# Performance work log

Hardware: AMD Instinct MI355X
Metric: run time of the kernel (lower is better)

Reference implementation:

```python
import jax, jax.numpy as jnp
import numpy as np

NTYPES = 2
B, N, MNEI = 4, 512, 100
M = MNEI * NTYPES          # neighbor slots = maxNeighborNum * ntypes
EMB_LAST = 100             # embedding net sizes [25, 50, 100]
FIT_H = 240
M2 = 16
RMIN, RMAX = 0.5, 6.0


def setup_inputs():
    key = jax.random.key(0)
    ks = jax.random.split(key, 24)
    r = jax.random.uniform(ks[0], (B, N, M), minval=0.6, maxval=7.0)
    v = jax.random.normal(ks[1], (B, N, M, 3))
    v = v / jnp.linalg.norm(v, axis=-1, keepdims=True)
    keep = jax.random.uniform(ks[2], (B, N, M)) < 0.7
    ImageDR = jnp.concatenate([r[..., None], r[..., None] * v], axis=-1)
    ImageDR = jnp.where(keep[..., None], ImageDR, 0.0).astype(jnp.float32)
    Imagetype_map = jax.random.randint(ks[3], (N,), 0, NTYPES)
    list_neigh = jax.random.randint(ks[4], (B, N, M), 0, N + 1)
    type_map = jnp.arange(NTYPES)
    davg = (0.01 * jax.random.normal(ks[5], (NTYPES, M, 4))).astype(jnp.float32)
    dstd = (1.0 + 0.1 * jax.random.uniform(ks[6], (NTYPES, M, 4))).astype(jnp.float32)

    def w(k, shape, fan):
        return (jax.random.normal(k, shape) / np.sqrt(fan)).astype(jnp.float32)

    def b(k, shape):
        return (0.1 * jax.random.normal(k, shape)).astype(jnp.float32)

    emb_W0 = w(ks[7], (NTYPES, NTYPES, 1, 25), 1)
    emb_b0 = b(ks[8], (NTYPES, NTYPES, 25))
    emb_W1 = w(ks[9], (NTYPES, NTYPES, 25, 50), 25)
    emb_b1 = b(ks[10], (NTYPES, NTYPES, 50))
    emb_W2 = w(ks[11], (NTYPES, NTYPES, 50, 100), 50)
    emb_b2 = b(ks[12], (NTYPES, NTYPES, 100))
    fin = M2 * EMB_LAST
    fit_W0 = w(ks[13], (NTYPES, fin, FIT_H), fin)
    fit_b0 = b(ks[14], (NTYPES, FIT_H))
    fit_W1 = w(ks[15], (NTYPES, FIT_H, FIT_H), FIT_H)
    fit_b1 = b(ks[16], (NTYPES, FIT_H))
    fit_W2 = w(ks[17], (NTYPES, FIT_H, FIT_H), FIT_H)
    fit_b2 = b(ks[18], (NTYPES, FIT_H))
    fit_W3 = w(ks[19], (NTYPES, FIT_H, 1), FIT_H)
    fit_b3 = b(ks[20], (NTYPES, 1))
    energy_shift = jnp.array([-3.37, -5.21], dtype=jnp.float32)
    return dict(list_neigh=list_neigh, Imagetype_map=Imagetype_map, type_map=type_map,
                ImageDR=ImageDR, nghost=0, davg=davg, dstd=dstd,
                emb_W0=emb_W0, emb_b0=emb_b0, emb_W1=emb_W1, emb_b1=emb_b1,
                emb_W2=emb_W2, emb_b2=emb_b2,
                fit_W0=fit_W0, fit_b0=fit_b0, fit_W1=fit_W1, fit_b1=fit_b1,
                fit_W2=fit_W2, fit_b2=fit_b2, fit_W3=fit_W3, fit_b3=fit_b3,
                energy_shift=energy_shift)


def _emb(s, W0, b0, W1, b1, W2, b2):
    # DeepPot-SE embedding net with doubling resnet connections
    h = jnp.tanh(s @ W0 + b0)                                   # [..., 25]
    h = jnp.tanh(h @ W1 + b1) + jnp.concatenate([h, h], -1)     # [..., 50]
    return jnp.tanh(h @ W2 + b2) + jnp.concatenate([h, h], -1)  # [..., 100]


def _fit(d, W0, b0, W1, b1, W2, b2, W3, b3):
    h = jnp.tanh(d @ W0 + b0)
    h = h + jnp.tanh(h @ W1 + b1)
    h = h + jnp.tanh(h @ W2 + b2)
    return h @ W3 + b3


def _forward(ImageDR, davg, dstd,
             emb_W0, emb_b0, emb_W1, emb_b1, emb_W2, emb_b2,
             fit_W0, fit_b0, fit_W1, fit_b1, fit_W2, fit_b2, fit_W3, fit_b3,
             energy_shift, Imagetype_map):
    Bsz, Nat, Mtot, _ = ImageDR.shape
    m = Mtot // NTYPES
    R = ImageDR[..., 0]
    Rsafe = jnp.where(R > 1e-5, R, 1.0)
    # smooth switching function s(r): 1/r below Rmin, polynomial taper to Rmax
    u = (R - RMIN) / (RMAX - RMIN)
    mid = (u ** 3 * (-6.0 * u * u + 15.0 * u - 10.0) + 1.0) / Rsafe
    S = jnp.where((R > 0) & (R < RMIN), 1.0 / Rsafe,
                  jnp.where((R > RMIN) & (R < RMAX), mid, 0.0))
    msk = (jnp.abs(R) > 1e-5)[..., None]
    Ri = jnp.concatenate([S[..., None],
                          jnp.where(msk, (S / Rsafe)[..., None] * ImageDR[..., 1:4], 0.0)],
                         axis=-1)                                    # [B,N,M,4] = (s, s*x/r, s*y/r, s*z/r)
    # per-center-type normalization (irregular gather of stats)
    Rn = (Ri - davg[Imagetype_map][None]) / dstd[Imagetype_map][None]
    tmask = [(Imagetype_map == i).astype(Rn.dtype)[None, :, None, None] for i in range(NTYPES)]
    xyz = jnp.zeros((Bsz, Nat, 4, EMB_LAST), Rn.dtype)
    for j in range(NTYPES):                                          # neighbor-type slice
        sl = Rn[:, :, j * m:(j + 1) * m, :]                          # [B,N,m,4]
        s = sl[..., 0:1]
        G = jnp.zeros(sl.shape[:3] + (EMB_LAST,), sl.dtype)
        for i in range(NTYPES):                                      # center type -> pair net (i, j)
            G = G + tmask[i] * _emb(s, emb_W0[i, j], emb_b0[i, j],
                                    emb_W1[i, j], emb_b1[i, j], emb_W2[i, j], emb_b2[i, j])
        xyz = xyz + jnp.einsum('bnmk,bnmc->bnkc', sl, G)
    xyz = xyz / (m * NTYPES)
    # descriptor D = (Ri^T G)^T (Ri^T G)[:, :M2], flattened -> [B,N,EMB_LAST*M2]
    D = jnp.einsum('bnkc,bnkd->bncd', xyz, xyz[..., :M2]).reshape(Bsz, Nat, -1)
    Ei = jnp.zeros((Bsz, Nat), D.dtype)
    for i in range(NTYPES):
        e = _fit(D, fit_W0[i], fit_b0[i], fit_W1[i], fit_b1[i],
                 fit_W2[i], fit_b2[i], fit_W3[i], fit_b3[i])[..., 0] + energy_shift[i]
        Ei = Ei + tmask[i][:, :, 0, 0] * e
    Etot = jnp.sum(Ei, axis=1)
    return Etot, Ei


def reference(list_neigh, Imagetype_map, type_map, ImageDR, nghost, davg, dstd,
              emb_W0, emb_b0, emb_W1, emb_b1, emb_W2, emb_b2,
              fit_W0, fit_b0, fit_W1, fit_b1, fit_W2, fit_b2, fit_W3, fit_b3,
              energy_shift):
    return _forward(ImageDR, davg, dstd,
                    emb_W0, emb_b0, emb_W1, emb_b1, emb_W2, emb_b2,
                    fit_W0, fit_b0, fit_W1, fit_b1, fit_W2, fit_b2, fit_W3, fit_b3,
                    energy_shift, Imagetype_map)
```

## Files before the change

### kernel.cpp

```cpp
#include <hip/hip_runtime.h>
#include <math.h>

#define NT 2
#define BSZ 4
#define NAT 512
#define NATOMS 2048
#define NNEI 200
#define EMB 100
#define FITH 240
#define DDIM 1600
#define TBK 1024

#define BIAS_F  16
#define W3C_F   (BIAS_F + 3 * 512)
#define PERM_I  2064
#define CNT_I   (PERM_I + 2064)
#define IPERM_I (CNT_I + 4)
#define DONE_I  (IPERM_I + 2048)
#define USH_BYTE 24832
#define TBL_U   0
#define W0T_U   409600
#define W1T_U   (W0T_U + 819200)
#define W2T_U   (W1T_U + 262144)
#define D_U     (W2T_U + 262144)
#define D_SZ    (129 * 50 * 512)
#define USH_END (D_U + D_SZ)
#define WS_NEED ((size_t)USH_BYTE + (size_t)USH_END * 2)

#define N_W0 819200
#define N_W1 262144
#define N_W2 262144
#define N_B  1536
#define N_W3 512
#define N_EI 2048
#define N_WT (N_W0 + N_W1 + N_W2 + N_B + N_W3 + N_EI)
#define WT_BLK ((N_WT + 255) / 256)
#define TB_BLK 512

#define HPAD 264
#define FIT_NBLK 256

typedef short s8v __attribute__((ext_vector_type(8)));
typedef float f4v __attribute__((ext_vector_type(4)));

__device__ __forceinline__ float ftanh(float x) {
    float ax = fabsf(x);
    float e = __expf(2.0f * ax);
    float t = 1.0f - __fdividef(2.0f, e + 1.0f);
    return (x < 0.0f) ? -t : t;
}
__device__ __forceinline__ unsigned short f2bf(float f) {
    unsigned u = __float_as_uint(f);
    u += 0x7FFFu + ((u >> 16) & 1u);
    return (unsigned short)(u >> 16);
}
__device__ __forceinline__ float bf2f(unsigned short s) {
    return __uint_as_float(((unsigned)s) << 16);
}
__device__ __forceinline__ float calc_S(float R) {
    float Rsafe = (R > 1e-5f) ? R : 1.0f;
    float u = (R - 0.5f) * (1.0f / 5.5f);
    float uu = u * u;
    float mid = (u * uu * (-6.0f * uu + 15.0f * u - 10.0f) + 1.0f) / Rsafe;
    float S = 0.0f;
    if (R > 0.0f && R < 0.5f)      S = 1.0f / Rsafe;
    else if (R > 0.5f && R < 6.0f) S = mid;
    return S;
}

__global__ void __launch_bounds__(256) prep_kernel(
    const float* __restrict__ fW0, const float* __restrict__ fW1,
    const float* __restrict__ fW2,
    const float* __restrict__ fb0, const float* __restrict__ fb1,
    const float* __restrict__ fb2,
    const float* __restrict__ fW3, const float* __restrict__ fb3,
    const float* __restrict__ eshift,
    const float* __restrict__ davg, const float* __restrict__ dstd,
    const float* __restrict__ eW0, const float* __restrict__ eb0,
    const float* __restrict__ eW1, const float* __restrict__ eb1,
    const float* __restrict__ eW2, const float* __restrict__ eb2,
    const int* __restrict__ itype,
    float* __restrict__ ws, float* __restrict__ out)
{
    __shared__ float los[100], his[100];
    __shared__ float rng[2];
    __shared__ float h0s[8][25];
    __shared__ float h1s[8][50];
    __shared__ int pcnt, poff0, poff1;
    const int tid = threadIdx.x;
    int bxg = blockIdx.x;
    unsigned short* u0 = (unsigned short*)((char*)ws + USH_BYTE);

    if (bxg < WT_BLK) {
        int id = bxg * 256 + tid;
        if (id < N_W0) {
            int e = id & 7, lane = (id >> 3) & 63;
            int rem = id >> 9;
            int kt = rem % 50, c16 = rem / 50;
            int n = c16 * 16 + (lane & 15);
            int k = kt * 32 + (lane >> 4) * 8 + e;
            float v = 0.0f;
            if (n < 240)                  v = fW0[(size_t)k * 240 + n];
            else if (n >= 256 && n < 496) v = fW0[(size_t)(1600 + k) * 240 + (n - 256)];
            u0[W0T_U + id] = f2bf(v);
            return;
        }
        id -= N_W0;
        if (id < N_W1) {
            int e = id & 7, lane = (id >> 3) & 63;
            int rem = id >> 9;
            int kt = rem & 15, c16 = rem >> 4;
            int n = c16 * 16 + (lane & 15);
            int k = kt * 32 + (lane >> 4) * 8 + e;
            float v = 0.0f;
            if (n < 240 && k < 240)       v = fW1[(size_t)k * 240 + n];
            else if (n >= 256 && n < 496 && k >= 256 && k < 496)
                                          v = fW1[(size_t)(240 + (k - 256)) * 240 + (n - 256)];
            u0[W1T_U + id] = f2bf(v);
            return;
        }
        id -= N_W1;
        if (id < N_W2) {
            int e = id & 7, lane = (id >> 3) & 63;
            int rem = id >> 9;
            int kt = rem & 15, c16 = rem >> 4;
            int n = c16 * 16 + (lane & 15);
            int k = kt * 32 + (lane >> 4) * 8 + e;
            float v = 0.0f;
            if (n < 240 && k < 240)       v = fW2[(size_t)k * 240 + n];
            else if (n >= 256 && n < 496 && k >= 256 && k < 496)
                                          v = fW2[(size_t)(240 + (k - 256)) * 240 + (n - 256)];
            u0[W2T_U + id] = f2bf(v);
            return;
        }
        id -= N_W2;
        if (id < N_B) {
            int l = id / 512, n = id - l * 512;
            const float* fb = (l == 0) ? fb0 : (l == 1) ? fb1 : fb2;
            float v = 0.0f;
            if (n < 240)                  v = fb[n];
            else if (n >= 256 && n < 496) v = fb[240 + (n - 256)];
            ws[BIAS_F + l * 512 + n] = v;
            return;
        }
        id -= N_B;
        if (id < N_W3) {
            int n = id;
            float v = 0.0f;
            if (n < 240)                  v = fW3[n];
            else if (n >= 256 && n < 496) v = fW3[240 + (n - 256)];
            ws[W3C_F + n] = v;
            return;
        }
        id -= N_W3;
        if (id < N_EI) {
            int t = itype[id & (NAT - 1)];
            out[4 + id] = fb3[t] + eshift[t];
        }
        return;
    }
    bxg -= WT_BLK;
    if (bxg < TB_BLK) {
        const int nid = bxg >> 7;
        const int kb  = (bxg & 127) * 8;
        const int t = nid >> 1, j = nid & 1;
        if (tid < 100) {
            int m = j * 100 + tid;
            float av = davg[(t * NNEI + m) * 4];
            float sd = dstd[(t * NNEI + m) * 4];
            float inv = __fdividef(1.0f, sd);
            float a = (0.0f - av) * inv;
            float b = (2.0f - av) * inv;
            los[tid] = fminf(a, b);
            his[tid] = fmaxf(a, b);
        }
        __syncthreads();
        if (tid == 0) {
            float lo = los[0], hi = his[0];
            for (int i = 1; i < 100; ++i) { lo = fminf(lo, los[i]); hi = fmaxf(hi, his[i]); }
            rng[0] = lo; rng[1] = hi - lo;
            if (kb == 0) {
                ws[nid * 2] = lo;
                ws[nid * 2 + 1] = (float)(TBK - 1) / (hi - lo);
            }
        }
        __syncthreads();
        const float smin = rng[0], span = rng[1];
        const float* W0 = eW0 + nid * 25;
        const float* B0 = eb0 + nid * 25;
        if (tid < 200) {
            int q = tid / 25, a = tid % 25;
            float s = smin + span * ((float)(kb + q) * (1.0f / (TBK - 1)));
            h0s[q][a] = ftanh(fmaf(s, W0[a], B0[a]));
        }
        __syncthreads();
        const float* W1 = eW1 + nid * 1250;
        const float* B1 = eb1 + nid * 50;
        for (int idx = tid; idx < 400; idx += 256) {
            int q = idx / 50, cc = idx % 50;
            float acc = B1[cc];
#pragma unroll
            for (int a = 0; a < 25; ++a) acc = fmaf(h0s[q][a], W1[a * 50 + cc], acc);
            h1s[q][cc] = ftanh(acc) + h0s[q][(cc < 25) ? cc : cc - 25];
        }
        __syncthreads();
        const float* W2 = eW2 + nid * 5000;
        const float* B2 = eb2 + nid * 100;
        unsigned short* tblu = u0 + TBL_U;
        for (int idx = tid; idx < 800; idx += 256) {
            int q = idx / 100, c = idx % 100;
            float acc = B2[c];
#pragma unroll
            for (int a = 0; a < 50; ++a) acc = fmaf(h1s[q][a], W2[a * 100 + c], acc);
            float g = ftanh(acc) + h1s[q][(c < 50) ? c : c - 50];
            tblu[(size_t)(nid * TBK + kb + q) * 100 + c] = f2bf(g);
        }
        return;
    }
    if (tid == 0) { pcnt = 0; poff0 = 0; poff1 = 0; }
    __syncthreads();
    int* wsi = (int*)ws;
    int local0 = 0;
    for (int i = tid; i < NATOMS; i += 256) local0 += (itype[i & (NAT - 1)] == 0);
    atomicAdd(&pcnt, local0);
    __syncthreads();
    const int c0 = pcnt;
    const int c0p = (c0 + 15) & ~15;
    for (int i = tid; i < NATOMS; i += 256) {
        int t = itype[i & (NAT - 1)];
        int pos = (t == 0) ? atomicAdd(&poff0, 1) : (c0p + atomicAdd(&poff1, 1));
        wsi[PERM_I + pos] = i;
        wsi[IPERM_I + i] = pos;
    }
    if (tid == 0) {
        wsi[CNT_I] = c0; wsi[CNT_I + 1] = NATOMS - c0; wsi[CNT_I + 2] = c0p;
        wsi[DONE_I] = 0;
    }
}

__global__ void __launch_bounds__(512) embed_kernel(
    const int* __restrict__ itype, const float* __restrict__ imagedr,
    const float* __restrict__ davg, const float* __restrict__ dstd,
    float* __restrict__ ws)
{
    __shared__ __align__(16) float4 srn[NNEI];
    __shared__ float sx[NNEI];
    __shared__ float part[8][400];
    const int atom = blockIdx.x;
    const int n = atom & (NAT - 1);
    const int tid = threadIdx.x;
    const int t = itype[n];
    unsigned short* u0 = (unsigned short*)((char*)ws + USH_BYTE);
    const int* wsi = (const int*)ws;

    const float sm0 = ws[(t * 2 + 0) * 2], sc0 = ws[(t * 2 + 0) * 2 + 1];
    const float sm1 = ws[(t * 2 + 1) * 2], sc1 = ws[(t * 2 + 1) * 2 + 1];

    for (int m = tid; m < NNEI; m += 512) {
        float4 dr = ((const float4*)imagedr)[(size_t)atom * NNEI + m];
        float R = dr.x;
        float S = calc_S(R);
        float Rsafe = (R > 1e-5f) ? R : 1.0f;
        float sr = (fabsf(R) > 1e-5f) ? (S / Rsafe) : 0.0f;
        float4 av = ((const float4*)davg)[t * NNEI + m];
        float4 sd = ((const float4*)dstd)[t * NNEI + m];
        float4 rv;
        rv.x = (S         - av.x) / sd.x;
        rv.y = (sr * dr.y - av.y) / sd.y;
        rv.z = (sr * dr.z - av.z) / sd.z;
        rv.w = (sr * dr.w - av.w) / sd.w;
        srn[m] = rv;
        float smin = (m >= 100) ? sm1 : sm0;
        float scal = (m >= 100) ? sc1 : sc0;
        sx[m] = fminf(fmaxf((rv.x - smin) * scal, 0.0f), (float)(TBK - 2) + 0.9999f);
    }
    __syncthreads();

    const int v = tid >> 6, lane = tid & 63;
    const int w = v >> 2;
    const int seg = v & 3;
    const unsigned short* T = u0 + TBL_U + (size_t)(t * 2 + w) * TBK * EMB;
    const bool act = (lane < 50);
    float xE0 = 0, xE1 = 0, xE2 = 0, xE3 = 0;
    float xO0 = 0, xO1 = 0, xO2 = 0, xO3 = 0;
#pragma unroll 5
    for (int mi = seg * 25; mi < seg * 25 + 25; ++mi) {
        int m = w * 100 + mi;
        float4 rv = srn[m];
        float x = sx[m];
        int i = (int)x;
        float f = x - (float)i;
        const unsigned short* Tr = T + (size_t)i * EMB;
        unsigned r0 = act ? *(const unsigned*)(Tr + 2 * lane) : 0u;
        unsigned r1 = act ? *(const unsigned*)(Tr + EMB + 2 * lane) : 0u;
        float g0e = bf2f((unsigned short)(r0 & 0xFFFFu));
        float g0o = bf2f((unsigned short)(r0 >> 16));
        float g1e = bf2f((unsigned short)(r1 & 0xFFFFu));
        float g1o = bf2f((unsigned short)(r1 >> 16));
        float ge = fmaf(f, g1e - g0e, g0e);
        float go = fmaf(f, g1o - g0o, g0o);
        xE0 = fmaf(rv.x, ge, xE0); xE1 = fmaf(rv.y, ge, xE1);
        xE2 = fmaf(rv.z, ge, xE2); xE3 = fmaf(rv.w, ge, xE3);
        xO0 = fmaf(rv.x, go, xO0); xO1 = fmaf(rv.y, go, xO1);
        xO2 = fmaf(rv.z, go, xO2); xO3 = fmaf(rv.w, go, xO3);
    }
    if (act) {
        const int c = 2 * lane;
        part[v][0 * 100 + c] = xE0; part[v][0 * 100 + c + 1] = xO0;
        part[v][1 * 100 + c] = xE1; part[v][1 * 100 + c + 1] = xO1;
        part[v][2 * 100 + c] = xE2; part[v][2 * 100 + c + 1] = xO2;
        part[v][3 * 100 + c] = xE3; part[v][3 * 100 + c + 1] = xO3;
    }
    __syncthreads();
    const float inv = 1.0f / 200.0f;
    for (int idx = tid; idx < 400; idx += 512) {
        float s = 0.0f;
#pragma unroll
        for (int pv = 0; pv < 8; ++pv) s += part[pv][idx];
        part[0][idx] = s * inv;
    }
    __syncthreads();
    const int p = wsi[IPERM_I + atom];
    const int rb = p >> 4, mrp = p & 15;
    unsigned short* Df = u0 + D_U;
    const float* xt = part[0];
    for (int k8 = tid; k8 < 200; k8 += 512) {
        int k = k8 * 8;
        int c = k >> 4, d0 = k & 15;
        int kt = k >> 5, q = (k >> 3) & 3;
        s8v pack;
#pragma unroll
        for (int e = 0; e < 8; ++e) {
            int d = d0 + e;
            float s = xt[c] * xt[d] + xt[100 + c] * xt[100 + d]
                    + xt[200 + c] * xt[200 + d] + xt[300 + c] * xt[300 + d];
            ((unsigned short*)&pack)[e] = f2bf(s);
        }
        *(s8v*)(Df + ((size_t)(rb * 50 + kt) * 64 + q * 16 + mrp) * 8) = pack;
    }
}

__global__ void __launch_bounds__(512, 2) fit_kernel(
    const unsigned short* __restrict__ Af,
    const unsigned short* __restrict__ W0F,
    const unsigned short* __restrict__ W1F,
    const unsigned short* __restrict__ W2F,
    const float* __restrict__ biases,
    const float* __restrict__ w3c,
    int* __restrict__ wsi,
    float* __restrict__ out)
{
    __shared__ float lred[4][64][17];
    __shared__ unsigned short Hs0[16 * HPAD];
    __shared__ unsigned short Hs1[16 * HPAD];
    __shared__ float red2[16][4];
    __shared__ int lastFlag;
    __shared__ float er[8];

    const int z = blockIdx.y;
    const int cnt = wsi[CNT_I + z];
    const int my = blockIdx.x;
    const int tid = threadIdx.x;
    const bool work = (my * 16 < cnt);
    if (work) {
        const int basep = z ? wsi[CNT_I + 2] : 0;
        const int w = tid >> 6, lane = tid & 63;
        const int mr = lane & 15, q = lane >> 4;
        const int wc = w & 3, h = w >> 2;
        const int n0 = z * 256 + wc * 64;
        const int m0 = my * 16;
        const int rb = (basep >> 4) + my;
        const int c16b = z * 16 + wc * 4;

        f4v a0 = {0,0,0,0}, a1 = {0,0,0,0}, a2 = {0,0,0,0}, a3 = {0,0,0,0};
        {
            const unsigned short* Ap = Af  + ((size_t)(rb * 50 + h * 25) * 64 + lane) * 8;
            const unsigned short* Bp = W0F + ((size_t)(c16b * 50 + h * 25) * 64 + lane) * 8;
#pragma unroll
            for (int kt = 0; kt < 25; ++kt) {
                s8v av = *(const s8v*)(Ap + kt * 512);
                s8v b0 = *(const s8v*)(Bp + kt * 512);
                s8v b1 = *(const s8v*)(Bp + 25600 + kt * 512);
                s8v b2 = *(const s8v*)(Bp + 51200 + kt * 512);
                s8v b3 = *(const s8v*)(Bp + 76800 + kt * 512);
                a0 = __builtin_amdgcn_mfma_f32_16x16x32_bf16(av, b0, a0, 0, 0, 0);
                a1 = __builtin_amdgcn_mfma_f32_16x16x32_bf16(av, b1, a1, 0, 0, 0);
                a2 = __builtin_amdgcn_mfma_f32_16x16x32_bf16(av, b2, a2, 0, 0, 0);
                a3 = __builtin_amdgcn_mfma_f32_16x16x32_bf16(av, b3, a3, 0, 0, 0);
            }
        }
        if (h == 1) {
#pragma unroll
            for (int r = 0; r < 4; ++r) {
                lred[wc][lane][r]      = a0[r];
                lred[wc][lane][4 + r]  = a1[r];
                lred[wc][lane][8 + r]  = a2[r];
                lred[wc][lane][12 + r] = a3[r];
            }
        }
        __syncthreads();
        if (h == 0) {
#pragma unroll
            for (int j = 0; j < 4; ++j) {
                const float bv = biases[n0 + j * 16 + mr];
                f4v* ap = (j == 0) ? &a0 : (j == 1) ? &a1 : (j == 2) ? &a2 : &a3;
                const int col = wc * 64 + j * 16 + mr;
#pragma unroll
                for (int r = 0; r < 4; ++r) {
                    float s = (*ap)[r] + lred[wc][lane][j * 4 + r] + bv;
                    int row = q * 4 + r;
                    Hs0[row * HPAD + col] = f2bf(ftanh(s));
                }
            }
        }
        __syncthreads();

        {
            const unsigned short* Bp = W1F + ((size_t)(c16b * 16 + z * 8 + h * 4) * 64 + lane) * 8;
            f4v ac[4] = {{0,0,0,0},{0,0,0,0},{0,0,0,0},{0,0,0,0}};
#pragma unroll
            for (int kt = 0; kt < 4; ++kt) {
                s8v av = *(const s8v*)((const char*)Hs0
                         + (size_t)mr * (HPAD * 2) + h * 256 + q * 16 + kt * 64);
                s8v b0 = *(const s8v*)(Bp + kt * 512);
                s8v b1 = *(const s8v*)(Bp + 8192 + kt * 512);
                s8v b2 = *(const s8v*)(Bp + 16384 + kt * 512);
                s8v b3 = *(const s8v*)(Bp + 24576 + kt * 512);
                ac[0] = __builtin_amdgcn_mfma_f32_16x16x32_bf16(av, b0, ac[0], 0, 0, 0);
                ac[1] = __builtin_amdgcn_mfma_f32_16x16x32_bf16(av, b1, ac[1], 0, 0, 0);
                ac[2] = __builtin_amdgcn_mfma_f32_16x16x32_bf16(av, b2, ac[2], 0, 0, 0);
                ac[3] = __builtin_amdgcn_mfma_f32_16x16x32_bf16(av, b3, ac[3], 0, 0, 0);
            }
            if (h == 1) {
#pragma unroll
                for (int j = 0; j < 4; ++j)
#pragma unroll
                    for (int r = 0; r < 4; ++r) lred[wc][lane][j * 4 + r] = ac[j][r];
            }
            __syncthreads();
            if (h == 0) {
#pragma unroll
                for (int j = 0; j < 4; ++j) {
                    const float bv = biases[512 + n0 + j * 16 + mr];
                    const int col = wc * 64 + j * 16 + mr;
#pragma unroll
                    for (int r = 0; r < 4; ++r) {
                        float s = ac[j][r] + lred[wc][lane][j * 4 + r] + bv;
                        int row = q * 4 + r;
                        float hv = bf2f(Hs0[row * HPAD + col]) + ftanh(s);
                        Hs1[row * HPAD + col] = f2bf(hv);
                    }
                }
            }
            __syncthreads();
        }

        {
            const unsigned short* Bp = W2F + ((size_t)(c16b * 16 + z * 8 + h * 4) * 64 + lane) * 8;
            f4v ac[4] = {{0,0,0,0},{0,0,0,0},{0,0,0,0},{0,0,0,0}};
#pragma unroll
            for (int kt = 0; kt < 4; ++kt) {
                s8v av = *(const s8v*)((const char*)Hs1
                         + (size_t)mr * (HPAD * 2) + h * 256 + q * 16 + kt * 64);
                s8v b0 = *(const s8v*)(Bp + kt * 512);
                s8v b1 = *(const s8v*)(Bp + 8192 + kt * 512);
                s8v b2 = *(const s8v*)(Bp + 16384 + kt * 512);
                s8v b3 = *(const s8v*)(Bp + 24576 + kt * 512);
                ac[0] = __builtin_amdgcn_mfma_f32_16x16x32_bf16(av, b0, ac[0], 0, 0, 0);
                ac[1] = __builtin_amdgcn_mfma_f32_16x16x32_bf16(av, b1, ac[1], 0, 0, 0);
                ac[2] = __builtin_amdgcn_mfma_f32_16x16x32_bf16(av, b2, ac[2], 0, 0, 0);
                ac[3] = __builtin_amdgcn_mfma_f32_16x16x32_bf16(av, b3, ac[3], 0, 0, 0);
            }
            if (h == 1) {
#pragma unroll
                for (int j = 0; j < 4; ++j)
#pragma unroll
                    for (int r = 0; r < 4; ++r) lred[wc][lane][j * 4 + r] = ac[j][r];
            }
            __syncthreads();
            if (h == 0) {
                float pr[4] = {0, 0, 0, 0};
#pragma unroll
                for (int j = 0; j < 4; ++j) {
                    const int col = n0 + j * 16 + mr;
                    const float bv = biases[1024 + col];
                    const float wv = w3c[col];
                    const int coll = wc * 64 + j * 16 + mr;
#pragma unroll
                    for (int r = 0; r < 4; ++r) {
                        float s = ac[j][r] + lred[wc][lane][j * 4 + r] + bv;
                        int row = q * 4 + r;
                        float hv = bf2f(Hs1[row * HPAD + coll]) + ftanh(s);
                        pr[r] = fmaf(hv, wv, pr[r]);
                    }
                }
#pragma unroll
                for (int r = 0; r < 4; ++r) {
                    float p = pr[r];
                    p += __shfl_xor(p, 1, 16);
                    p += __shfl_xor(p, 2, 16);
                    p += __shfl_xor(p, 4, 16);
                    p += __shfl_xor(p, 8, 16);
                    if (mr == 0) red2[q * 4 + r][wc] = p;
                }
            }
            __syncthreads();
            if (tid < 16 && m0 + tid < cnt) {
                const int orow = wsi[PERM_I + basep + m0 + tid];
                out[4 + orow] += red2[tid][0] + red2[tid][1] + red2[tid][2] + red2[tid][3];
            }
        }
    }

    __syncthreads();
    if (tid == 0) {
        __threadfence();
        int prev = atomicAdd(&wsi[DONE_I], 1);
        lastFlag = (prev == FIT_NBLK - 1);
    }
    __syncthreads();
    if (lastFlag) {
        __threadfence();
        const int g = tid >> 7, l = tid & 127;
        float s = 0.0f;
        for (int nn = l; nn < NAT; nn += 128) s += out[4 + g * NAT + nn];
#pragma unroll
        for (int off = 32; off > 0; off >>= 1) s += __shfl_down(s, off, 64);
        if ((l & 63) == 0) er[g * 2 + (l >> 6)] = s;
        __syncthreads();
        if (tid < 4) out[tid] = er[tid * 2] + er[tid * 2 + 1];
    }
}

__global__ void etot_kernel(float* __restrict__ out) {
    const int b = blockIdx.x;
    float s = 0.0f;
    for (int n = threadIdx.x; n < NAT; n += 256) s += out[4 + b * NAT + n];
#pragma unroll
    for (int off = 32; off > 0; off >>= 1) s += __shfl_down(s, off, 64);
    __shared__ float rr[4];
    if ((threadIdx.x & 63) == 0) rr[threadIdx.x >> 6] = s;
    __syncthreads();
    if (threadIdx.x == 0) out[b] = rr[0] + rr[1] + rr[2] + rr[3];
}

__global__ void dp_atom_kernel(
    const int* __restrict__ itype, const float* __restrict__ imagedr,
    const float* __restrict__ davg, const float* __restrict__ dstd,
    const float* __restrict__ eW0, const float* __restrict__ eb0,
    const float* __restrict__ eW1, const float* __restrict__ eb1,
    const float* __restrict__ eW2, const float* __restrict__ eb2,
    const float* __restrict__ fW0, const float* __restrict__ fb0,
    const float* __restrict__ fW1, const float* __restrict__ fb1,
    const float* __restrict__ fW2, const float* __restrict__ fb2,
    const float* __restrict__ fW3, const float* __restrict__ fb3,
    const float* __restrict__ eshift, float* __restrict__ out)
{
    __shared__ __align__(16) float4 rn4[NNEI];
    __shared__ __align__(16) float  xyz[4 * EMB];
    __shared__ __align__(16) float  h0s[100 * 25];
    __shared__ __align__(16) float  smem[100 * 52];
    const int atom = blockIdx.x;
    const int n = atom & (NAT - 1);
    const int tid = threadIdx.x;
    const int t = itype[n];
    for (int m = tid; m < NNEI; m += 256) {
        float4 dr = ((const float4*)imagedr)[(size_t)atom * NNEI + m];
        float R = dr.x;
        float S = calc_S(R);
        float Rsafe = (R > 1e-5f) ? R : 1.0f;
        float sr = (fabsf(R) > 1e-5f) ? (S / Rsafe) : 0.0f;
        float4 av = ((const float4*)davg)[t * NNEI + m];
        float4 sd = ((const float4*)dstd)[t * NNEI + m];
        float4 rv;
        rv.x = (S - av.x) / sd.x; rv.y = (sr * dr.y - av.y) / sd.y;
        rv.z = (sr * dr.z - av.z) / sd.z; rv.w = (sr * dr.w - av.w) / sd.w;
        rn4[m] = rv;
    }
    const int c = tid & 127; const int mh = tid >> 7;
    float xp0 = 0, xp1 = 0, xp2 = 0, xp3 = 0;
    for (int j = 0; j < NT; ++j) {
        const int wb = t * NT + j;
        const float* W0 = eW0 + wb * 25; const float* B0 = eb0 + wb * 25;
        const float* W1 = eW1 + wb * 1250; const float* B1 = eb1 + wb * 50;
        const float* W2 = eW2 + wb * 5000; const float* B2 = eb2 + wb * 100;
        __syncthreads();
        for (int idx = tid; idx < 2500; idx += 256) {
            int m = idx / 25, a = idx - m * 25;
            h0s[idx] = ftanh(fmaf(rn4[j * 100 + m].x, W0[a], B0[a]));
        }
        __syncthreads();
        for (int idx = tid; idx < 5000; idx += 256) {
            int m = idx / 50, cc = idx - m * 50;
            const float* h0m = h0s + m * 25;
            float acc = B1[cc];
#pragma unroll
            for (int a = 0; a < 25; ++a) acc = fmaf(h0m[a], W1[a * 50 + cc], acc);
            smem[m * 52 + cc] = ftanh(acc) + h0m[(cc < 25) ? cc : cc - 25];
        }
        for (int idx = tid; idx < 200; idx += 256)
            smem[(idx >> 1) * 52 + 50 + (idx & 1)] = 0.0f;
        __syncthreads();
        if (c < EMB) {
            float w2c[52];
#pragma unroll
            for (int a = 0; a < 50; ++a) w2c[a] = W2[a * EMB + c];
            w2c[50] = 0; w2c[51] = 0;
            const float bc = B2[c];
            const int sk = (c < 50) ? c : c - 50;
            for (int i = 0; i < 50; ++i) {
                int m = mh * 50 + i;
                const float* h1m = smem + m * 52;
                float acc = bc;
#pragma unroll
                for (int q = 0; q < 13; ++q) {
                    float4 hv = ((const float4*)h1m)[q];
                    acc = fmaf(hv.x, w2c[4 * q], acc); acc = fmaf(hv.y, w2c[4 * q + 1], acc);
                    acc = fmaf(hv.z, w2c[4 * q + 2], acc); acc = fmaf(hv.w, w2c[4 * q + 3], acc);
                }
                float g = ftanh(acc) + h1m[sk];
                float4 rm = rn4[j * 100 + m];
                xp0 = fmaf(rm.x, g, xp0); xp1 = fmaf(rm.y, g, xp1);
                xp2 = fmaf(rm.z, g, xp2); xp3 = fmaf(rm.w, g, xp3);
            }
        }
    }
    __syncthreads();
    const float inv = 1.0f / 200.0f;
    if (mh == 0 && c < EMB) {
        xyz[c] = xp0 * inv; xyz[EMB + c] = xp1 * inv;
        xyz[2 * EMB + c] = xp2 * inv; xyz[3 * EMB + c] = xp3 * inv;
    }
    __syncthreads();
    if (mh == 1 && c < EMB) {
        xyz[c] += xp0 * inv; xyz[EMB + c] += xp1 * inv;
        xyz[2 * EMB + c] += xp2 * inv; xyz[3 * EMB + c] += xp3 * inv;
    }
    __syncthreads();
    float* Dld = smem;
    for (int idx = tid; idx < DDIM; idx += 256) {
        int cc = idx >> 4, d = idx & 15;
        Dld[idx] = xyz[cc] * xyz[d] + xyz[EMB + cc] * xyz[EMB + d]
                 + xyz[2 * EMB + cc] * xyz[2 * EMB + d] + xyz[3 * EMB + cc] * xyz[3 * EMB + d];
    }
    __syncthreads();
    float* hA = smem + DDIM; float* hB = hA + FITH; float* h2 = hB + FITH; float* red = h2 + FITH;
    if (tid < FITH) {
        const float* W = fW0 + (size_t)t * DDIM * FITH;
        float acc = fb0[t * FITH + tid];
        for (int f = 0; f < DDIM; f += 4) {
            float4 dv = *(const float4*)(Dld + f);
            acc = fmaf(dv.x, W[f * FITH + tid], acc); acc = fmaf(dv.y, W[(f + 1) * FITH + tid], acc);
            acc = fmaf(dv.z, W[(f + 2) * FITH + tid], acc); acc = fmaf(dv.w, W[(f + 3) * FITH + tid], acc);
        }
        hA[tid] = ftanh(acc);
    }
    __syncthreads();
    if (tid < FITH) {
        const float* W = fW1 + t * FITH * FITH;
        float acc = fb1[t * FITH + tid];
        for (int f = 0; f < FITH; f += 4) {
            float4 hv = *(const float4*)(hA + f);
            acc = fmaf(hv.x, W[f * FITH + tid], acc); acc = fmaf(hv.y, W[(f + 1) * FITH + tid], acc);
            acc = fmaf(hv.z, W[(f + 2) * FITH + tid], acc); acc = fmaf(hv.w, W[(f + 3) * FITH + tid], acc);
        }
        hB[tid] = hA[tid] + ftanh(acc);
    }
    __syncthreads();
    if (tid < FITH) {
        const float* W = fW2 + t * FITH * FITH;
        float acc = fb2[t * FITH + tid];
        for (int f = 0; f < FITH; f += 4) {
            float4 hv = *(const float4*)(hB + f);
            acc = fmaf(hv.x, W[f * FITH + tid], acc); acc = fmaf(hv.y, W[(f + 1) * FITH + tid], acc);
            acc = fmaf(hv.z, W[(f + 2) * FITH + tid], acc); acc = fmaf(hv.w, W[(f + 3) * FITH + tid], acc);
        }
        h2[tid] = hB[tid] + ftanh(acc);
    }
    __syncthreads();
    float p = (tid < FITH) ? h2[tid] * fW3[t * FITH + tid] : 0.0f;
#pragma unroll
    for (int off = 32; off > 0; off >>= 1) p += __shfl_down(p, off, 64);
    if ((tid & 63) == 0) red[tid >> 6] = p;
    __syncthreads();
    if (tid == 0) out[4 + atom] = red[0] + red[1] + red[2] + red[3] + fb3[t] + eshift[t];
}

extern "C" void kernel_launch(void* const* d_in, const int* in_sizes, int n_in,
                              void* d_out, int out_size, void* d_ws, size_t ws_size,
                              hipStream_t stream) {
    const int*   itype   = (const int*)  d_in[1];
    const float* imagedr = (const float*)d_in[3];
    const float* davg    = (const float*)d_in[5];
    const float* dstd    = (const float*)d_in[6];
    const float* eW0     = (const float*)d_in[7];
    const float* eb0     = (const float*)d_in[8];
    const float* eW1     = (const float*)d_in[9];
    const float* eb1     = (const float*)d_in[10];
    const float* eW2     = (const float*)d_in[11];
    const float* eb2     = (const float*)d_in[12];
    const float* fW0     = (const float*)d_in[13];
    const float* fb0     = (const float*)d_in[14];
    const float* fW1     = (const float*)d_in[15];
    const float* fb1     = (const float*)d_in[16];
    const float* fW2     = (const float*)d_in[17];
    const float* fb2     = (const float*)d_in[18];
    const float* fW3     = (const float*)d_in[19];
    const float* fb3     = (const float*)d_in[20];
    const float* eshift  = (const float*)d_in[21];
    float* out = (float*)d_out;
    float* ws  = (float*)d_ws;

    if (ws_size >= WS_NEED) {
        unsigned short* u0 = (unsigned short*)((char*)ws + USH_BYTE);
        int* wsi = (int*)ws;
        prep_kernel<<<WT_BLK + TB_BLK + 1, 256, 0, stream>>>(
            fW0, fW1, fW2, fb0, fb1, fb2, fW3, fb3, eshift,
            davg, dstd, eW0, eb0, eW1, eb1, eW2, eb2, itype, ws, out);
        embed_kernel<<<NATOMS, 512, 0, stream>>>(itype, imagedr, davg, dstd, ws);
        fit_kernel<<<dim3(128, 2), 512, 0, stream>>>(
            u0 + D_U, u0 + W0T_U, u0 + W1T_U, u0 + W2T_U,
            ws + BIAS_F, ws + W3C_F, wsi, out);
    } else {
        dp_atom_kernel<<<NATOMS, 256, 0, stream>>>(itype, imagedr, davg, dstd,
            eW0, eb0, eW1, eb1, eW2, eb2,
            fW0, fb0, fW1, fb1, fW2, fb2, fW3, fb3, eshift, out);
        etot_kernel<<<BSZ, 256, 0, stream>>>(out);
    }
}
```

Baseline: 167.5 us.

## Split fitting-net GEMMs along K across all waves with LDS atomic reduction

Each of the 8 waves now computes all 16 output column tiles over its own slice of K, instead of 4 column groups with a 2-way K split. Partial sums are combined through float atomicAdd into a shared 16x264 buffer, and the epilogue (bias, tanh, residual, final dot) is spread evenly over all 512 threads. The goal is to reuse each A fragment across 16 MFMAs and to balance the epilogue work. In exchange each wave holds 64 accumulator registers, and the change adds LDS atomic contention plus an extra zero-fill pass.

```diff
diff --git a/kernel.cpp b/kernel.cpp
--- a/kernel.cpp
+++ b/kernel.cpp
@@ -350,10 +350,10 @@
     int* __restrict__ wsi,
     float* __restrict__ out)
 {
-    __shared__ float lred[4][64][17];
+    __shared__ float S[16][264];
     __shared__ unsigned short Hs0[16 * HPAD];
     __shared__ unsigned short Hs1[16 * HPAD];
-    __shared__ float red2[16][4];
+    __shared__ float red2[16];
     __shared__ int lastFlag;
     __shared__ float er[8];
 
@@ -364,151 +364,120 @@
     const bool work = (my * 16 < cnt);
     if (work) {
         const int basep = z ? wsi[CNT_I + 2] : 0;
-        const int w = tid >> 6, lane = tid & 63;
+        const int v = tid >> 6, lane = tid & 63;
         const int mr = lane & 15, q = lane >> 4;
-        const int wc = w & 3, h = w >> 2;
-        const int n0 = z * 256 + wc * 64;
+        const int rb = (basep >> 4) + my;
         const int m0 = my * 16;
-        const int rb = (basep >> 4) + my;
-        const int c16b = z * 16 + wc * 4;
-
-        f4v a0 = {0,0,0,0}, a1 = {0,0,0,0}, a2 = {0,0,0,0}, a3 = {0,0,0,0};
+        const int erow = tid >> 5, ec0 = (tid & 31) * 8;
+
         {
-            const unsigned short* Ap = Af  + ((size_t)(rb * 50 + h * 25) * 64 + lane) * 8;
-            const unsigned short* Bp = W0F + ((size_t)(c16b * 50 + h * 25) * 64 + lane) * 8;
-#pragma unroll
-            for (int kt = 0; kt < 25; ++kt) {
-                s8v av = *(const s8v*)(Ap + kt * 512);
-                s8v b0 = *(const s8v*)(Bp + kt * 512);
-                s8v b1 = *(const s8v*)(Bp + 25600 + kt * 512);
-                s8v b2 = *(const s8v*)(Bp + 51200 + kt * 512);
-                s8v b3 = *(const s8v*)(Bp + 76800 + kt * 512);
-                a0 = __builtin_amdgcn_mfma_f32_16x16x32_bf16(av, b0, a0, 0, 0, 0);
-                a1 = __builtin_amdgcn_mfma_f32_16x16x32_bf16(av, b1, a1, 0, 0, 0);
-                a2 = __builtin_amdgcn_mfma_f32_16x16x32_bf16(av, b2, a2, 0, 0, 0);
-                a3 = __builtin_amdgcn_mfma_f32_16x16x32_bf16(av, b3, a3, 0, 0, 0);
-            }
-        }
-        if (h == 1) {
-#pragma unroll
-            for (int r = 0; r < 4; ++r) {
-                lred[wc][lane][r]      = a0[r];
-                lred[wc][lane][4 + r]  = a1[r];
-                lred[wc][lane][8 + r]  = a2[r];
-                lred[wc][lane][12 + r] = a3[r];
-            }
-        }
-        __syncthreads();
-        if (h == 0) {
-#pragma unroll
-            for (int j = 0; j < 4; ++j) {
-                const float bv = biases[n0 + j * 16 + mr];
-                f4v* ap = (j == 0) ? &a0 : (j == 1) ? &a1 : (j == 2) ? &a2 : &a3;
-                const int col = wc * 64 + j * 16 + mr;
-#pragma unroll
-                for (int r = 0; r < 4; ++r) {
-                    float s = (*ap)[r] + lred[wc][lane][j * 4 + r] + bv;
-                    int row = q * 4 + r;
-                    Hs0[row * HPAD + col] = f2bf(ftanh(s));
+            float* Sf = &S[0][0];
+            for (int i = tid; i < 16 * 264; i += 512) Sf[i] = 0.0f;
+        }
+        __syncthreads();
+
+        {
+            const int lo = v * 6 + min(v, 2);
+            const int nk = (v < 2) ? 7 : 6;
+            f4v acc[16];
+#pragma unroll
+            for (int j = 0; j < 16; ++j) acc[j] = (f4v){0.f, 0.f, 0.f, 0.f};
+            const unsigned short* Ab = Af  + ((size_t)(rb * 50 + lo) * 64 + lane) * 8;
+            const unsigned short* Bb = W0F + ((size_t)((z * 16) * 50 + lo) * 64 + lane) * 8;
+            for (int kk = 0; kk < nk; ++kk) {
+                s8v av = *(const s8v*)(Ab + kk * 512);
+#pragma unroll
+                for (int j = 0; j < 16; ++j) {
+                    s8v b = *(const s8v*)(Bb + (size_t)j * 25600 + kk * 512);
+                    acc[j] = __builtin_amdgcn_mfma_f32_16x16x32_bf16(av, b, acc[j], 0, 0, 0);
                 }
             }
-        }
-        __syncthreads();
-
+#pragma unroll
+            for (int j = 0; j < 16; ++j)
+#pragma unroll
+                for (int r = 0; r < 4; ++r)
+                    atomicAdd(&S[q * 4 + r][j * 16 + mr], acc[j][r]);
+        }
+        __syncthreads();
         {
-            const unsigned short* Bp = W1F + ((size_t)(c16b * 16 + z * 8 + h * 4) * 64 + lane) * 8;
-            f4v ac[4] = {{0,0,0,0},{0,0,0,0},{0,0,0,0},{0,0,0,0}};
-#pragma unroll
-            for (int kt = 0; kt < 4; ++kt) {
-                s8v av = *(const s8v*)((const char*)Hs0
-                         + (size_t)mr * (HPAD * 2) + h * 256 + q * 16 + kt * 64);
-                s8v b0 = *(const s8v*)(Bp + kt * 512);
-                s8v b1 = *(const s8v*)(Bp + 8192 + kt * 512);
-                s8v b2 = *(const s8v*)(Bp + 16384 + kt * 512);
-                s8v b3 = *(const s8v*)(Bp + 24576 + kt * 512);
-                ac[0] = __builtin_amdgcn_mfma_f32_16x16x32_bf16(av, b0, ac[0], 0, 0, 0);
-                ac[1] = __builtin_amdgcn_mfma_f32_16x16x32_bf16(av, b1, ac[1], 0, 0, 0);
-                ac[2] = __builtin_amdgcn_mfma_f32_16x16x32_bf16(av, b2, ac[2], 0, 0, 0);
-                ac[3] = __builtin_amdgcn_mfma_f32_16x16x32_bf16(av, b3, ac[3], 0, 0, 0);
-            }
-            if (h == 1) {
-#pragma unroll
-                for (int j = 0; j < 4; ++j)
-#pragma unroll
-                    for (int r = 0; r < 4; ++r) lred[wc][lane][j * 4 + r] = ac[j][r];
-            }
-            __syncthreads();
-            if (h == 0) {
-#pragma unroll
-                for (int j = 0; j < 4; ++j) {
-                    const float bv = biases[512 + n0 + j * 16 + mr];
-                    const int col = wc * 64 + j * 16 + mr;
-#pragma unroll
-                    for (int r = 0; r < 4; ++r) {
-                        float s = ac[j][r] + lred[wc][lane][j * 4 + r] + bv;
-                        int row = q * 4 + r;
-                        float hv = bf2f(Hs0[row * HPAD + col]) + ftanh(s);
-                        Hs1[row * HPAD + col] = f2bf(hv);
-                    }
-                }
-            }
-            __syncthreads();
-        }
+#pragma unroll
+            for (int e = 0; e < 8; ++e) {
+                int col = ec0 + e;
+                float s = S[erow][col] + biases[z * 256 + col];
+                Hs0[erow * HPAD + col] = f2bf(ftanh(s));
+                S[erow][col] = 0.0f;
+            }
+        }
+        __syncthreads();
 
         {
-            const unsigned short* Bp = W2F + ((size_t)(c16b * 16 + z * 8 + h * 4) * 64 + lane) * 8;
-            f4v ac[4] = {{0,0,0,0},{0,0,0,0},{0,0,0,0},{0,0,0,0}};
-#pragma unroll
-            for (int kt = 0; kt < 4; ++kt) {
-                s8v av = *(const s8v*)((const char*)Hs1
-                         + (size_t)mr * (HPAD * 2) + h * 256 + q * 16 + kt * 64);
-                s8v b0 = *(const s8v*)(Bp + kt * 512);
-                s8v b1 = *(const s8v*)(Bp + 8192 + kt * 512);
-                s8v b2 = *(const s8v*)(Bp + 16384 + kt * 512);
-                s8v b3 = *(const s8v*)(Bp + 24576 + kt * 512);
-                ac[0] = __builtin_amdgcn_mfma_f32_16x16x32_bf16(av, b0, ac[0], 0, 0, 0);
-                ac[1] = __builtin_amdgcn_mfma_f32_16x16x32_bf16(av, b1, ac[1], 0, 0, 0);
-                ac[2] = __builtin_amdgcn_mfma_f32_16x16x32_bf16(av, b2, ac[2], 0, 0, 0);
-                ac[3] = __builtin_amdgcn_mfma_f32_16x16x32_bf16(av, b3, ac[3], 0, 0, 0);
-            }
-            if (h == 1) {
-#pragma unroll
-                for (int j = 0; j < 4; ++j)
-#pragma unroll
-                    for (int r = 0; r < 4; ++r) lred[wc][lane][j * 4 + r] = ac[j][r];
-            }
-            __syncthreads();
-            if (h == 0) {
-                float pr[4] = {0, 0, 0, 0};
-#pragma unroll
-                for (int j = 0; j < 4; ++j) {
-                    const int col = n0 + j * 16 + mr;
-                    const float bv = biases[1024 + col];
-                    const float wv = w3c[col];
-                    const int coll = wc * 64 + j * 16 + mr;
-#pragma unroll
-                    for (int r = 0; r < 4; ++r) {
-                        float s = ac[j][r] + lred[wc][lane][j * 4 + r] + bv;
-                        int row = q * 4 + r;
-                        float hv = bf2f(Hs1[row * HPAD + coll]) + ftanh(s);
-                        pr[r] = fmaf(hv, wv, pr[r]);
-                    }
-                }
-#pragma unroll
-                for (int r = 0; r < 4; ++r) {
-                    float p = pr[r];
-                    p += __shfl_xor(p, 1, 16);
-                    p += __shfl_xor(p, 2, 16);
-                    p += __shfl_xor(p, 4, 16);
-                    p += __shfl_xor(p, 8, 16);
-                    if (mr == 0) red2[q * 4 + r][wc] = p;
-                }
-            }
-            __syncthreads();
-            if (tid < 16 && m0 + tid < cnt) {
-                const int orow = wsi[PERM_I + basep + m0 + tid];
-                out[4 + orow] += red2[tid][0] + red2[tid][1] + red2[tid][2] + red2[tid][3];
-            }
+            f4v acc[16];
+#pragma unroll
+            for (int j = 0; j < 16; ++j) acc[j] = (f4v){0.f, 0.f, 0.f, 0.f};
+            s8v av = *(const s8v*)((const char*)Hs0 + (size_t)mr * (HPAD * 2) + v * 64 + q * 16);
+            const unsigned short* Bb = W1F + ((size_t)((z * 16) * 16 + z * 8 + v) * 64 + lane) * 8;
+#pragma unroll
+            for (int j = 0; j < 16; ++j) {
+                s8v b = *(const s8v*)(Bb + (size_t)j * 8192);
+                acc[j] = __builtin_amdgcn_mfma_f32_16x16x32_bf16(av, b, acc[j], 0, 0, 0);
+            }
+#pragma unroll
+            for (int j = 0; j < 16; ++j)
+#pragma unroll
+                for (int r = 0; r < 4; ++r)
+                    atomicAdd(&S[q * 4 + r][j * 16 + mr], acc[j][r]);
+        }
+        __syncthreads();
+        {
+#pragma unroll
+            for (int e = 0; e < 8; ++e) {
+                int col = ec0 + e;
+                float s = S[erow][col] + biases[512 + z * 256 + col];
+                float hv = bf2f(Hs0[erow * HPAD + col]) + ftanh(s);
+                Hs1[erow * HPAD + col] = f2bf(hv);
+                S[erow][col] = 0.0f;
+            }
+        }
+        __syncthreads();
+
+        {
+            f4v acc[16];
+#pragma unroll
+            for (int j = 0; j < 16; ++j) acc[j] = (f4v){0.f, 0.f, 0.f, 0.f};
+            s8v av = *(const s8v*)((const char*)Hs1 + (size_t)mr * (HPAD * 2) + v * 64 + q * 16);
+            const unsigned short* Bb = W2F + ((size_t)((z * 16) * 16 + z * 8 + v) * 64 + lane) * 8;
+#pragma unroll
+            for (int j = 0; j < 16; ++j) {
+                s8v b = *(const s8v*)(Bb + (size_t)j * 8192);
+                acc[j] = __builtin_amdgcn_mfma_f32_16x16x32_bf16(av, b, acc[j], 0, 0, 0);
+            }
+#pragma unroll
+            for (int j = 0; j < 16; ++j)
+#pragma unroll
+                for (int r = 0; r < 4; ++r)
+                    atomicAdd(&S[q * 4 + r][j * 16 + mr], acc[j][r]);
+        }
+        __syncthreads();
+        {
+            float p = 0.0f;
+#pragma unroll
+            for (int e = 0; e < 8; ++e) {
+                int col = ec0 + e;
+                float s = S[erow][col] + biases[1024 + z * 256 + col];
+                float hv = bf2f(Hs1[erow * HPAD + col]) + ftanh(s);
+                p = fmaf(hv, w3c[z * 256 + col], p);
+            }
+            p += __shfl_xor(p, 1, 32);
+            p += __shfl_xor(p, 2, 32);
+            p += __shfl_xor(p, 4, 32);
+            p += __shfl_xor(p, 8, 32);
+            p += __shfl_xor(p, 16, 32);
+            if ((tid & 31) == 0) red2[erow] = p;
+        }
+        __syncthreads();
+        if (tid < 16 && m0 + tid < cnt) {
+            const int orow = wsi[PERM_I + basep + m0 + tid];
+            out[4 + orow] += red2[tid];
         }
     }
 
```

New measurement: 289.7 us. 1.73x slower.

## Split fit kernel K-reduction across four wave groups with 1024-thread blocks

Applied to the files above, without the earlier changes.

Doubles the fit kernel block to 1024 threads and splits each layer's K dimension over four wave groups instead of two (13/13/12/12 k-tiles for layer 0, two k-tiles each for layers 1 and 2). Partial sums from three groups go through a larger shared reduction buffer, and the final energy reduction is adapted to the new thread count. The goal is shorter per-wave serial MFMA chains and more latency hiding per block. The cost is more shared-memory reduction traffic, lower occupancy per CU, and a loop that is no longer fully unrolled.

```diff
diff --git a/kernel.cpp b/kernel.cpp
--- a/kernel.cpp
+++ b/kernel.cpp
@@ -340,7 +340,7 @@
     }
 }
 
-__global__ void __launch_bounds__(512, 2) fit_kernel(
+__global__ void __launch_bounds__(1024, 1) fit_kernel(
     const unsigned short* __restrict__ Af,
     const unsigned short* __restrict__ W0F,
     const unsigned short* __restrict__ W1F,
@@ -350,12 +350,12 @@
     int* __restrict__ wsi,
     float* __restrict__ out)
 {
-    __shared__ float lred[4][64][17];
+    __shared__ float lred[4][64][49];
     __shared__ unsigned short Hs0[16 * HPAD];
     __shared__ unsigned short Hs1[16 * HPAD];
     __shared__ float red2[16][4];
     __shared__ int lastFlag;
-    __shared__ float er[8];
+    __shared__ float er[16];
 
     const int z = blockIdx.y;
     const int cnt = wsi[CNT_I + z];
@@ -364,9 +364,9 @@
     const bool work = (my * 16 < cnt);
     if (work) {
         const int basep = z ? wsi[CNT_I + 2] : 0;
-        const int w = tid >> 6, lane = tid & 63;
+        const int v = tid >> 6, lane = tid & 63;
         const int mr = lane & 15, q = lane >> 4;
-        const int wc = w & 3, h = w >> 2;
+        const int wc = v & 3, h = v >> 2;
         const int n0 = z * 256 + wc * 64;
         const int m0 = my * 16;
         const int rb = (basep >> 4) + my;
@@ -374,10 +374,11 @@
 
         f4v a0 = {0,0,0,0}, a1 = {0,0,0,0}, a2 = {0,0,0,0}, a3 = {0,0,0,0};
         {
-            const unsigned short* Ap = Af  + ((size_t)(rb * 50 + h * 25) * 64 + lane) * 8;
-            const unsigned short* Bp = W0F + ((size_t)(c16b * 50 + h * 25) * 64 + lane) * 8;
-#pragma unroll
-            for (int kt = 0; kt < 25; ++kt) {
+            const int lo = h * 12 + min(h, 2);
+            const int nk = (h < 2) ? 13 : 12;
+            const unsigned short* Ap = Af  + ((size_t)(rb * 50 + lo) * 64 + lane) * 8;
+            const unsigned short* Bp = W0F + ((size_t)(c16b * 50 + lo) * 64 + lane) * 8;
+            for (int kt = 0; kt < nk; ++kt) {
                 s8v av = *(const s8v*)(Ap + kt * 512);
                 s8v b0 = *(const s8v*)(Bp + kt * 512);
                 s8v b1 = *(const s8v*)(Bp + 25600 + kt * 512);
@@ -389,13 +390,14 @@
                 a3 = __builtin_amdgcn_mfma_f32_16x16x32_bf16(av, b3, a3, 0, 0, 0);
             }
         }
-        if (h == 1) {
+        if (h > 0) {
+            const int s = (h - 1) * 16;
 #pragma unroll
             for (int r = 0; r < 4; ++r) {
-                lred[wc][lane][r]      = a0[r];
-                lred[wc][lane][4 + r]  = a1[r];
-                lred[wc][lane][8 + r]  = a2[r];
-                lred[wc][lane][12 + r] = a3[r];
+                lred[wc][lane][s + r]      = a0[r];
+                lred[wc][lane][s + 4 + r]  = a1[r];
+                lred[wc][lane][s + 8 + r]  = a2[r];
+                lred[wc][lane][s + 12 + r] = a3[r];
             }
         }
         __syncthreads();
@@ -407,7 +409,9 @@
                 const int col = wc * 64 + j * 16 + mr;
 #pragma unroll
                 for (int r = 0; r < 4; ++r) {
-                    float s = (*ap)[r] + lred[wc][lane][j * 4 + r] + bv;
+                    float s = (*ap)[r] + lred[wc][lane][j * 4 + r]
+                            + lred[wc][lane][16 + j * 4 + r]
+                            + lred[wc][lane][32 + j * 4 + r] + bv;
                     int row = q * 4 + r;
                     Hs0[row * HPAD + col] = f2bf(ftanh(s));
                 }
@@ -416,12 +420,12 @@
         __syncthreads();
 
         {
-            const unsigned short* Bp = W1F + ((size_t)(c16b * 16 + z * 8 + h * 4) * 64 + lane) * 8;
+            const unsigned short* Bp = W1F + ((size_t)(c16b * 16 + z * 8 + h * 2) * 64 + lane) * 8;
             f4v ac[4] = {{0,0,0,0},{0,0,0,0},{0,0,0,0},{0,0,0,0}};
 #pragma unroll
-            for (int kt = 0; kt < 4; ++kt) {
+            for (int kt = 0; kt < 2; ++kt) {
                 s8v av = *(const s8v*)((const char*)Hs0
-                         + (size_t)mr * (HPAD * 2) + h * 256 + q * 16 + kt * 64);
+                         + (size_t)mr * (HPAD * 2) + (h * 2 + kt) * 64 + q * 16);
                 s8v b0 = *(const s8v*)(Bp + kt * 512);
                 s8v b1 = *(const s8v*)(Bp + 8192 + kt * 512);
                 s8v b2 = *(const s8v*)(Bp + 16384 + kt * 512);
@@ -431,11 +435,12 @@
                 ac[2] = __builtin_amdgcn_mfma_f32_16x16x32_bf16(av, b2, ac[2], 0, 0, 0);
                 ac[3] = __builtin_amdgcn_mfma_f32_16x16x32_bf16(av, b3, ac[3], 0, 0, 0);
             }
-            if (h == 1) {
+            if (h > 0) {
+                const int s = (h - 1) * 16;
 #pragma unroll
                 for (int j = 0; j < 4; ++j)
 #pragma unroll
-                    for (int r = 0; r < 4; ++r) lred[wc][lane][j * 4 + r] = ac[j][r];
+                    for (int r = 0; r < 4; ++r) lred[wc][lane][s + j * 4 + r] = ac[j][r];
             }
             __syncthreads();
             if (h == 0) {
@@ -445,7 +450,9 @@
                     const int col = wc * 64 + j * 16 + mr;
 #pragma unroll
                     for (int r = 0; r < 4; ++r) {
-                        float s = ac[j][r] + lred[wc][lane][j * 4 + r] + bv;
+                        float s = ac[j][r] + lred[wc][lane][j * 4 + r]
+                                + lred[wc][lane][16 + j * 4 + r]
+                                + lred[wc][lane][32 + j * 4 + r] + bv;
                         int row = q * 4 + r;
                         float hv = bf2f(Hs0[row * HPAD + col]) + ftanh(s);
                         Hs1[row * HPAD + col] = f2bf(hv);
@@ -456,12 +463,12 @@
         }
 
         {
-            const unsigned short* Bp = W2F + ((size_t)(c16b * 16 + z * 8 + h * 4) * 64 + lane) * 8;
+            const unsigned short* Bp = W2F + ((size_t)(c16b * 16 + z * 8 + h * 2) * 64 + lane) * 8;
             f4v ac[4] = {{0,0,0,0},{0,0,0,0},{0,0,0,0},{0,0,0,0}};
 #pragma unroll
-            for (int kt = 0; kt < 4; ++kt) {
+            for (int kt = 0; kt < 2; ++kt) {
                 s8v av = *(const s8v*)((const char*)Hs1
-                         + (size_t)mr * (HPAD * 2) + h * 256 + q * 16 + kt * 64);
+                         + (size_t)mr * (HPAD * 2) + (h * 2 + kt) * 64 + q * 16);
                 s8v b0 = *(const s8v*)(Bp + kt * 512);
                 s8v b1 = *(const s8v*)(Bp + 8192 + kt * 512);
                 s8v b2 = *(const s8v*)(Bp + 16384 + kt * 512);
@@ -471,11 +478,12 @@
                 ac[2] = __builtin_amdgcn_mfma_f32_16x16x32_bf16(av, b2, ac[2], 0, 0, 0);
                 ac[3] = __builtin_amdgcn_mfma_f32_16x16x32_bf16(av, b3, ac[3], 0, 0, 0);
             }
-            if (h == 1) {
+            if (h > 0) {
+                const int s = (h - 1) * 16;
 #pragma unroll
                 for (int j = 0; j < 4; ++j)
 #pragma unroll
-                    for (int r = 0; r < 4; ++r) lred[wc][lane][j * 4 + r] = ac[j][r];
+                    for (int r = 0; r < 4; ++r) lred[wc][lane][s + j * 4 + r] = ac[j][r];
             }
             __syncthreads();
             if (h == 0) {
@@ -488,7 +496,9 @@
                     const int coll = wc * 64 + j * 16 + mr;
 #pragma unroll
                     for (int r = 0; r < 4; ++r) {
-                        float s = ac[j][r] + lred[wc][lane][j * 4 + r] + bv;
+                        float s = ac[j][r] + lred[wc][lane][j * 4 + r]
+                                + lred[wc][lane][16 + j * 4 + r]
+                                + lred[wc][lane][32 + j * 4 + r] + bv;
                         int row = q * 4 + r;
                         float hv = bf2f(Hs1[row * HPAD + coll]) + ftanh(s);
                         pr[r] = fmaf(hv, wv, pr[r]);
@@ -521,14 +531,15 @@
     __syncthreads();
     if (lastFlag) {
         __threadfence();
-        const int g = tid >> 7, l = tid & 127;
+        const int g = tid >> 8, l = tid & 255;
         float s = 0.0f;
-        for (int nn = l; nn < NAT; nn += 128) s += out[4 + g * NAT + nn];
+        for (int nn = l; nn < NAT; nn += 256) s += out[4 + g * NAT + nn];
 #pragma unroll
         for (int off = 32; off > 0; off >>= 1) s += __shfl_down(s, off, 64);
-        if ((l & 63) == 0) er[g * 2 + (l >> 6)] = s;
-        __syncthreads();
-        if (tid < 4) out[tid] = er[tid * 2] + er[tid * 2 + 1];
+        if ((l & 63) == 0) er[g * 4 + (l >> 6)] = s;
+        __syncthreads();
+        if (tid < 4)
+            out[tid] = er[tid * 4] + er[tid * 4 + 1] + er[tid * 4 + 2] + er[tid * 4 + 3];
     }
 }
 
@@ -718,7 +729,7 @@
             fW0, fW1, fW2, fb0, fb1, fb2, fW3, fb3, eshift,
             davg, dstd, eW0, eb0, eW1, eb1, eW2, eb2, itype, ws, out);
         embed_kernel<<<NATOMS, 512, 0, stream>>>(itype, imagedr, davg, dstd, ws);
-        fit_kernel<<<dim3(128, 2), 512, 0, stream>>>(
+        fit_kernel<<<dim3(128, 2), 1024, 0, stream>>>(
             u0 + D_U, u0 + W0T_U, u0 + W1T_U, u0 + W2T_U,
             ws + BIAS_F, ws + W3C_F, wsi, out);
     } else {
```

Measured after the change: 168.8 us. Within noise of the previous version (+0.8%).
